# Optimization experiments

Measured on AMD Instinct MI355X. Metric: run time of the kernel, lower is better.

Reference implementation:

```python
import jax, jax.numpy as jnp
import numpy as np

B, L, K, D = 65536, 4, 1024, 512


def setup_inputs() -> dict:
    key = jax.random.key(0)
    k1, k2 = jax.random.split(key)
    z_e = jax.random.normal(k1, (B, D), dtype=jnp.float32)
    # torch init: uniform(-1/codebook_size, 1/codebook_size)
    codebooks = jax.random.uniform(k2, (L, K, D), dtype=jnp.float32,
                                   minval=-1.0 / K, maxval=1.0 / K)
    return {"z_e": z_e, "codebooks": codebooks}


def reference(z_e, codebooks):
    sg = jax.lax.stop_gradient

    def step(carry, cb):
        # carry: (residual [B,D], quantized_sum [B,D], vq_loss scalar); cb: [K,D]
        residual, qsum, loss = carry
        # squared euclidean distances [B,K]
        d2 = (jnp.sum(residual * residual, axis=1, keepdims=True)
              + jnp.sum(cb * cb, axis=1)
              - 2.0 * residual @ cb.T)
        idx = jnp.argmin(d2, axis=1)          # [B]
        q = cb[idx]                           # [B,D] gather
        loss = loss + jnp.mean((q - sg(residual)) ** 2) \
                    + jnp.mean((sg(q) - residual) ** 2)
        return (residual - q, qsum + q, loss), idx

    init = (z_e, jnp.zeros_like(z_e), jnp.float32(0.0))
    (residual, qsum, vq_loss), codes = jax.lax.scan(step, init, codebooks)
    # straight-through estimator
    z_q_st = z_e + sg(qsum - z_e)
    return z_q_st, codes, vq_loss
```

## Files before the change

kernel.cpp:

```cpp
#include <hip/hip_runtime.h>
#include <math.h>

#define NB 65536
#define ND 512
#define NK 1024
#define NL 4
#define THR 1e-3f

typedef __attribute__((ext_vector_type(8))) short short8;
typedef __attribute__((ext_vector_type(4))) float floatx4;

__device__ inline unsigned short bf16_rne(float x) {
  unsigned int u = __float_as_uint(x);
  unsigned int r = u + 0x7FFFu + ((u >> 16) & 1u);
  return (unsigned short)(r >> 16);
}

__global__ void cn_kernel(const float* __restrict__ cb, float* __restrict__ cn) {
  const int code = blockIdx.x;
  const float* row = cb + (size_t)code * ND;
  const int t = threadIdx.x;
  const float x = row[t];
  const float y = row[t + 256];
  double s = (double)x * x + (double)y * y;
  for (int off = 32; off > 0; off >>= 1) s += __shfl_down(s, off);
  __shared__ double part[4];
  if ((t & 63) == 0) part[t >> 6] = s;
  __syncthreads();
  if (t == 0) cn[code] = (float)(part[0] + part[1] + part[2] + part[3]);
}

__global__ void rn_kernel(const float* __restrict__ x, float* __restrict__ rn) {
  const int t = threadIdx.x;
  const int row = blockIdx.x * 2 + (t >> 7);
  const int c = (t & 127) << 2;
  const float4 v = *(const float4*)(x + (size_t)row * ND + c);
  double s = (double)v.x * v.x + (double)v.y * v.y + (double)v.z * v.z + (double)v.w * v.w;
  for (int off = 32; off > 0; off >>= 1) s += __shfl_down(s, off);
  __shared__ double part[4];
  if ((t & 63) == 0) part[t >> 6] = s;
  __syncthreads();
  if ((t & 127) == 0) rn[row] = (float)(part[t >> 6] + part[(t >> 6) + 1]);
}

__global__ __launch_bounds__(512, 2)
void argmin_mfma(const float* __restrict__ res,
                 const float* __restrict__ cb,
                 const float* __restrict__ rn,
                 const float* __restrict__ cn,
                 unsigned int* __restrict__ cnt,
                 unsigned int* __restrict__ cand) {
  __shared__ short A_hi[128][40];
  __shared__ short A_lo[128][40];
  __shared__ short B_hi[256][40];
  __shared__ short B_lo[256][40];
  __shared__ float minbuf[128][4];

  const int t = threadIdx.x;
  const int lane = t & 63;
  const int w = t >> 6;
  const int wr = w >> 2;
  const int wc = w & 3;
  const int q = lane >> 4;
  const int col16 = lane & 15;
  const int rowbase = (blockIdx.x >> 1) * 128;
  const int cbase = (blockIdx.x & 1) * 512;

  const int sa_row = t >> 2, sa_k = (t & 3) * 8;
  const int sb_row = t >> 1, sb_k = (t & 1) * 16;

  for (int nc = 0; nc < 2; ++nc) {
    floatx4 acc[4][4];
#pragma unroll
    for (int i = 0; i < 4; ++i)
#pragma unroll
      for (int j = 0; j < 4; ++j) acc[i][j] = (floatx4){0.f, 0.f, 0.f, 0.f};

    float4 fa0, fa1, fb[4];
    {
      const float* ap = res + (size_t)(rowbase + sa_row) * ND + sa_k;
      fa0 = *(const float4*)(ap);
      fa1 = *(const float4*)(ap + 4);
      const float* bp = cb + (size_t)(cbase + nc * 256 + sb_row) * ND + sb_k;
#pragma unroll
      for (int j = 0; j < 4; ++j) fb[j] = *(const float4*)(bp + 4 * j);
    }

    for (int kc = 0; kc < 16; ++kc) {
      __syncthreads();
      {
        float av[8] = {fa0.x, fa0.y, fa0.z, fa0.w, fa1.x, fa1.y, fa1.z, fa1.w};
        short8 h, l;
#pragma unroll
        for (int j = 0; j < 8; ++j) {
          unsigned short hb = bf16_rne(av[j]);
          float hf = __uint_as_float((unsigned int)hb << 16);
          h[j] = (short)hb;
          l[j] = (short)bf16_rne(av[j] - hf);
        }
        *(short8*)&A_hi[sa_row][sa_k] = h;
        *(short8*)&A_lo[sa_row][sa_k] = l;
        float bv[16];
#pragma unroll
        for (int j = 0; j < 4; ++j) {
          bv[4 * j + 0] = fb[j].x; bv[4 * j + 1] = fb[j].y;
          bv[4 * j + 2] = fb[j].z; bv[4 * j + 3] = fb[j].w;
        }
        short8 h0, l0, h1, l1;
#pragma unroll
        for (int j = 0; j < 8; ++j) {
          unsigned short hb = bf16_rne(bv[j]);
          float hf = __uint_as_float((unsigned int)hb << 16);
          h0[j] = (short)hb;
          l0[j] = (short)bf16_rne(bv[j] - hf);
          unsigned short hb1 = bf16_rne(bv[j + 8]);
          float hf1 = __uint_as_float((unsigned int)hb1 << 16);
          h1[j] = (short)hb1;
          l1[j] = (short)bf16_rne(bv[j + 8] - hf1);
        }
        *(short8*)&B_hi[sb_row][sb_k] = h0;
        *(short8*)&B_lo[sb_row][sb_k] = l0;
        *(short8*)&B_hi[sb_row][sb_k + 8] = h1;
        *(short8*)&B_lo[sb_row][sb_k + 8] = l1;
      }
      __syncthreads();
      if (kc + 1 < 16) {
        const float* ap = res + (size_t)(rowbase + sa_row) * ND + (kc + 1) * 32 + sa_k;
        fa0 = *(const float4*)(ap);
        fa1 = *(const float4*)(ap + 4);
        const float* bp = cb + (size_t)(cbase + nc * 256 + sb_row) * ND + (kc + 1) * 32 + sb_k;
#pragma unroll
        for (int j = 0; j < 4; ++j) fb[j] = *(const float4*)(bp + 4 * j);
      }
      short8 ahi[4], alo[4], bhi[4], blo[4];
#pragma unroll
      for (int ti = 0; ti < 4; ++ti) {
        const int m = wr * 64 + ti * 16 + col16;
        ahi[ti] = *(short8*)&A_hi[m][q * 8];
        alo[ti] = *(short8*)&A_lo[m][q * 8];
      }
#pragma unroll
      for (int tj = 0; tj < 4; ++tj) {
        const int n = wc * 64 + tj * 16 + col16;
        bhi[tj] = *(short8*)&B_hi[n][q * 8];
        blo[tj] = *(short8*)&B_lo[n][q * 8];
      }
#pragma unroll
      for (int ti = 0; ti < 4; ++ti)
#pragma unroll
        for (int tj = 0; tj < 4; ++tj) {
          acc[ti][tj] = __builtin_amdgcn_mfma_f32_16x16x32_bf16(ahi[ti], bhi[tj], acc[ti][tj], 0, 0, 0);
          acc[ti][tj] = __builtin_amdgcn_mfma_f32_16x16x32_bf16(alo[ti], bhi[tj], acc[ti][tj], 0, 0, 0);
          acc[ti][tj] = __builtin_amdgcn_mfma_f32_16x16x32_bf16(ahi[ti], blo[tj], acc[ti][tj], 0, 0, 0);
        }
    }

    float rnv[16], cnv[4];
#pragma unroll
    for (int ti = 0; ti < 4; ++ti)
#pragma unroll
      for (int v = 0; v < 4; ++v)
        rnv[ti * 4 + v] = rn[rowbase + wr * 64 + ti * 16 + q * 4 + v];
#pragma unroll
    for (int tj = 0; tj < 4; ++tj)
      cnv[tj] = cn[cbase + nc * 256 + wc * 64 + tj * 16 + col16];

    float rm[16];
#pragma unroll
    for (int ti = 0; ti < 4; ++ti)
#pragma unroll
      for (int v = 0; v < 4; ++v) {
        float m0 = INFINITY;
#pragma unroll
        for (int tj = 0; tj < 4; ++tj) {
          const float d2 = (rnv[ti * 4 + v] + cnv[tj]) - 2.0f * acc[ti][tj][v];
          m0 = fminf(m0, d2);
        }
        rm[ti * 4 + v] = m0;
      }
#pragma unroll
    for (int mask = 1; mask < 16; mask <<= 1)
#pragma unroll
      for (int i = 0; i < 16; ++i) rm[i] = fminf(rm[i], __shfl_xor(rm[i], mask));
    if (col16 == 0) {
#pragma unroll
      for (int ti = 0; ti < 4; ++ti)
#pragma unroll
        for (int v = 0; v < 4; ++v)
          minbuf[wr * 64 + ti * 16 + q * 4 + v][wc] = rm[ti * 4 + v];
    }
    __syncthreads();
    if (t < 128)
      minbuf[t][0] = fminf(fminf(minbuf[t][0], minbuf[t][1]), fminf(minbuf[t][2], minbuf[t][3]));
    __syncthreads();
#pragma unroll
    for (int ti = 0; ti < 4; ++ti)
#pragma unroll
      for (int v = 0; v < 4; ++v) {
        const int grow = rowbase + wr * 64 + ti * 16 + q * 4 + v;
        const float thrv = minbuf[wr * 64 + ti * 16 + q * 4 + v][0] + THR;
#pragma unroll
        for (int tj = 0; tj < 4; ++tj) {
          const float d2 = (rnv[ti * 4 + v] + cnv[tj]) - 2.0f * acc[ti][tj][v];
          if (d2 <= thrv) {
            const unsigned int gcol = cbase + nc * 256 + wc * 64 + tj * 16 + col16;
            const unsigned int slot = atomicAdd(&cnt[grow], 1u);
            if (slot < 16) cand[(size_t)grow * 16 + slot] = gcol;
          }
        }
      }
    __syncthreads();
  }
}

__global__ __launch_bounds__(256)
void recheck_kernel(const float* __restrict__ res, const float* __restrict__ cb,
                    const float* __restrict__ rn, const float* __restrict__ cn,
                    const unsigned int* __restrict__ cnt,
                    const unsigned int* __restrict__ cand,
                    int* __restrict__ idx) {
  const int t = threadIdx.x;
  const int lane = t & 63;
  const int slot = lane & 3;
  const int row = blockIdx.x * 64 + (t >> 2);
  const int wavebase = blockIdx.x * 64 + (t >> 6) * 16;
  const unsigned int c = cnt[row];
  const float* rp = res + (size_t)row * ND;
  const float rnr = rn[row];

  if (c <= 16) {
    float bestv = INFINITY;
    int bestk = 0x7fffffff;
    for (unsigned int s = slot; s < c; s += 4) {
      const int k = (int)cand[(size_t)row * 16 + s];
      const float* cp = cb + (size_t)k * ND;
      float acc = 0.f;
#pragma unroll 8
      for (int d = 0; d < ND; d += 4) {
        const float4 rv = *(const float4*)(rp + d);
        const float4 cv = *(const float4*)(cp + d);
        acc = fmaf(rv.x, cv.x, acc);
        acc = fmaf(rv.y, cv.y, acc);
        acc = fmaf(rv.z, cv.z, acc);
        acc = fmaf(rv.w, cv.w, acc);
      }
      const float d2 = (rnr + cn[k]) - 2.0f * acc;
      if (d2 < bestv || (d2 == bestv && k < bestk)) { bestv = d2; bestk = k; }
    }
#pragma unroll
    for (int off = 1; off < 4; off <<= 1) {
      const float ov = __shfl_xor(bestv, off);
      const int ok = __shfl_xor(bestk, off);
      if (ov < bestv || (ov == bestv && ok < bestk)) { bestv = ov; bestk = ok; }
    }
    if (slot == 0) idx[row] = bestk;
  }

  unsigned long long ovf = __ballot(slot == 0 && c > 16);
  while (ovf) {
    const int src = (int)__ffsll(ovf) - 1;
    ovf &= ovf - 1;
    const int orow = wavebase + (src >> 2);
    const float* orp = res + (size_t)orow * ND;
    const float ornr = rn[orow];
    float bv = INFINITY;
    int bk = 0x7fffffff;
    for (int kk = 0; kk < NK; kk += 64) {
      const int k = kk + lane;
      const float* cp = cb + (size_t)k * ND;
      float acc = 0.f;
      for (int d = 0; d < ND; d += 4) {
        const float4 rv = *(const float4*)(orp + d);
        const float4 cv = *(const float4*)(cp + d);
        acc = fmaf(rv.x, cv.x, acc);
        acc = fmaf(rv.y, cv.y, acc);
        acc = fmaf(rv.z, cv.z, acc);
        acc = fmaf(rv.w, cv.w, acc);
      }
      const float d2 = (ornr + cn[k]) - 2.0f * acc;
      if (d2 < bv || (d2 == bv && k < bk)) { bv = d2; bk = k; }
    }
    for (int off = 32; off > 0; off >>= 1) {
      const float ov = __shfl_down(bv, off);
      const int ok = __shfl_down(bk, off);
      if (ov < bv || (ov == bv && ok < bk)) { bv = ov; bk = ok; }
    }
    if (lane == 0) idx[orow] = bk;
  }
}

__global__ void update_kernel(const float* __restrict__ res_in,
                              const float* __restrict__ cb,
                              const int* __restrict__ idx,
                              float* __restrict__ res_out,
                              float* __restrict__ codes_out,
                              float* __restrict__ rn_out,
                              double* __restrict__ lacc) {
  const int t = threadIdx.x;
  const int row = blockIdx.x * 2 + (t >> 7);
  const int c = (t & 127) << 2;
  const int k = idx[row];
  const float4 r = *(const float4*)(res_in + (size_t)row * ND + c);
  const float4 q = *(const float4*)(cb + (size_t)k * ND + c);
  float4 nr;
  nr.x = r.x - q.x; nr.y = r.y - q.y; nr.z = r.z - q.z; nr.w = r.w - q.w;
  *(float4*)(res_out + (size_t)row * ND + c) = nr;
  if (c == 0) codes_out[row] = (float)k;
  double s = (double)nr.x * nr.x + (double)nr.y * nr.y +
             (double)nr.z * nr.z + (double)nr.w * nr.w;
  for (int off = 32; off > 0; off >>= 1) s += __shfl_down(s, off);
  __shared__ double part[4];
  if ((t & 63) == 0) part[t >> 6] = s;
  __syncthreads();
  if ((t & 127) == 0) rn_out[row] = (float)(part[t >> 6] + part[(t >> 6) + 1]);
  if (t == 0) atomicAdd(&lacc[blockIdx.x & 511], part[0] + part[1] + part[2] + part[3]);
}

__global__ void loss_reduce(const double* __restrict__ lacc, float* __restrict__ out) {
  const int t = threadIdx.x;
  double s = 0.0;
  for (int i = t; i < NL * 512; i += 256) s += lacc[i];
  for (int off = 32; off > 0; off >>= 1) s += __shfl_down(s, off);
  __shared__ double part[4];
  if ((t & 63) == 0) part[t >> 6] = s;
  __syncthreads();
  if (t == 0)
    out[(size_t)NB * ND + (size_t)NL * NB] =
        (float)(2.0 * (part[0] + part[1] + part[2] + part[3]) / ((double)NB * (double)ND));
}

__global__ void final_kernel(const float* __restrict__ z_e,
                             const float* __restrict__ cbs,
                             float* __restrict__ out) {
  const size_t gid = (size_t)blockIdx.x * 256 + threadIdx.x;
  const int row = (int)(gid >> 7);
  const int c = ((int)gid & 127) << 2;
  const float* codes = out + (size_t)NB * ND;
  const int k0 = (int)codes[0 * NB + row];
  const int k1 = (int)codes[1 * NB + row];
  const int k2 = (int)codes[2 * NB + row];
  const int k3 = (int)codes[3 * NB + row];
  const float4 q0 = *(const float4*)(cbs + ((size_t)0 * NK + k0) * ND + c);
  const float4 q1 = *(const float4*)(cbs + ((size_t)1 * NK + k1) * ND + c);
  const float4 q2 = *(const float4*)(cbs + ((size_t)2 * NK + k2) * ND + c);
  const float4 q3 = *(const float4*)(cbs + ((size_t)3 * NK + k3) * ND + c);
  const float4 z = *(const float4*)(z_e + (size_t)row * ND + c);
  float4 qs, o;
  qs.x = ((q0.x + q1.x) + q2.x) + q3.x;
  qs.y = ((q0.y + q1.y) + q2.y) + q3.y;
  qs.z = ((q0.z + q1.z) + q2.z) + q3.z;
  qs.w = ((q0.w + q1.w) + q2.w) + q3.w;
  o.x = z.x + (qs.x - z.x);
  o.y = z.y + (qs.y - z.y);
  o.z = z.z + (qs.z - z.z);
  o.w = z.w + (qs.w - z.w);
  *(float4*)(out + (size_t)row * ND + c) = o;
}

extern "C" void kernel_launch(void* const* d_in, const int* in_sizes, int n_in,
                              void* d_out, int out_size, void* d_ws, size_t ws_size,
                              hipStream_t stream) {
  const float* z_e = (const float*)d_in[0];
  const float* cbs = (const float*)d_in[1];
  float* out = (float*)d_out;
  char* ws = (char*)d_ws;

  double* lacc = (double*)ws;
  float* rn = (float*)(ws + 16384);
  float* cn = (float*)(ws + 16384 + 262144);
  unsigned int* cnt = (unsigned int*)(ws + 16384 + 262144 + 16384);
  unsigned int* cand = (unsigned int*)(ws + 16384 + 262144 + 16384 + 262144);
  int* idx = (int*)(ws + 16384 + 262144 + 16384 + 262144 + 4194304);

  float* resb = out;
  float* codes = out + (size_t)NB * ND;

  hipMemsetAsync(lacc, 0, NL * 512 * sizeof(double), stream);
  cn_kernel<<<NL * NK, 256, 0, stream>>>(cbs, cn);
  rn_kernel<<<NB / 2, 256, 0, stream>>>(z_e, rn);

  for (int l = 0; l < NL; ++l) {
    const float* rin = (l == 0) ? z_e : resb;
    const float* cbl = cbs + (size_t)l * NK * ND;
    hipMemsetAsync(cnt, 0, (size_t)NB * 4, stream);
    argmin_mfma<<<(NB / 128) * 2, 512, 0, stream>>>(rin, cbl, rn, cn + l * NK, cnt, cand);
    recheck_kernel<<<NB / 64, 256, 0, stream>>>(rin, cbl, rn, cn + l * NK, cnt, cand, idx);
    update_kernel<<<NB / 2, 256, 0, stream>>>(
        rin, cbl, idx, resb, codes + (size_t)l * NB, rn, lacc + (size_t)l * 512);
  }

  loss_reduce<<<1, 256, 0, stream>>>(lacc, out);
  final_kernel<<<(NB * (size_t)ND) / 4 / 256, 256, 0, stream>>>(z_e, cbs, out);
}
```

Before: 2.323 ms.

## Precompute bf16 hi/lo splits of codebook and residual outside the GEMM

Adds a split kernel that converts the codebooks into bf16 hi/lo arrays once. rn_kernel and update_kernel also emit bf16 hi/lo copies of the residual. The argmin MFMA kernel can then load pre-split shorts instead of converting fp32 on every tile. In the original code the codebook tile was re-split by each of the 1024 row blocks, so this removes redundant conversion ALU work and halves-per-array load bytes. The cost is extra workspace, extra writes in update/rn, and a mode choice that depends on the workspace size.

Result: no change. 2.342 ms (+0.8%).

```diff
diff --git a/kernel.cpp b/kernel.cpp
--- a/kernel.cpp
+++ b/kernel.cpp
@@ -8,6 +8,7 @@
 #define THR 1e-3f
 
 typedef __attribute__((ext_vector_type(8))) short short8;
+typedef __attribute__((ext_vector_type(4))) short short4_t;
 typedef __attribute__((ext_vector_type(4))) float floatx4;
 
 __device__ inline unsigned short bf16_rne(float x) {
@@ -30,22 +31,59 @@
   if (t == 0) cn[code] = (float)(part[0] + part[1] + part[2] + part[3]);
 }
 
-__global__ void rn_kernel(const float* __restrict__ x, float* __restrict__ rn) {
+__global__ void split_kernel(const float* __restrict__ x, short* __restrict__ hi,
+                             short* __restrict__ lo) {
+  const size_t i = ((size_t)blockIdx.x * 256 + threadIdx.x) * 4;
+  const float4 v = *(const float4*)(x + i);
+  const float av[4] = {v.x, v.y, v.z, v.w};
+  short4_t h, l;
+#pragma unroll
+  for (int j = 0; j < 4; ++j) {
+    unsigned short hb = bf16_rne(av[j]);
+    float hf = __uint_as_float((unsigned int)hb << 16);
+    h[j] = (short)hb;
+    l[j] = (short)bf16_rne(av[j] - hf);
+  }
+  *(short4_t*)(hi + i) = h;
+  *(short4_t*)(lo + i) = l;
+}
+
+__global__ void rn_kernel(const float* __restrict__ x, float* __restrict__ rn,
+                          short* __restrict__ rh, short* __restrict__ rl, int do_split) {
   const int t = threadIdx.x;
   const int row = blockIdx.x * 2 + (t >> 7);
   const int c = (t & 127) << 2;
-  const float4 v = *(const float4*)(x + (size_t)row * ND + c);
+  const size_t off = (size_t)row * ND + c;
+  const float4 v = *(const float4*)(x + off);
+  if (do_split) {
+    const float av[4] = {v.x, v.y, v.z, v.w};
+    short4_t h, l;
+#pragma unroll
+    for (int j = 0; j < 4; ++j) {
+      unsigned short hb = bf16_rne(av[j]);
+      float hf = __uint_as_float((unsigned int)hb << 16);
+      h[j] = (short)hb;
+      l[j] = (short)bf16_rne(av[j] - hf);
+    }
+    *(short4_t*)(rh + off) = h;
+    *(short4_t*)(rl + off) = l;
+  }
   double s = (double)v.x * v.x + (double)v.y * v.y + (double)v.z * v.z + (double)v.w * v.w;
-  for (int off = 32; off > 0; off >>= 1) s += __shfl_down(s, off);
+  for (int off2 = 32; off2 > 0; off2 >>= 1) s += __shfl_down(s, off2);
   __shared__ double part[4];
   if ((t & 63) == 0) part[t >> 6] = s;
   __syncthreads();
   if ((t & 127) == 0) rn[row] = (float)(part[t >> 6] + part[(t >> 6) + 1]);
 }
 
+template <int MODE>
 __global__ __launch_bounds__(512, 2)
 void argmin_mfma(const float* __restrict__ res,
+                 const short* __restrict__ rh,
+                 const short* __restrict__ rl,
                  const float* __restrict__ cb,
+                 const short* __restrict__ cbh,
+                 const short* __restrict__ cbl,
                  const float* __restrict__ rn,
                  const float* __restrict__ cn,
                  unsigned int* __restrict__ cnt,
@@ -77,18 +115,36 @@
       for (int j = 0; j < 4; ++j) acc[i][j] = (floatx4){0.f, 0.f, 0.f, 0.f};
 
     float4 fa0, fa1, fb[4];
+    short8 pah, pal, pbh0, pbh1, pbl0, pbl1;
     {
-      const float* ap = res + (size_t)(rowbase + sa_row) * ND + sa_k;
-      fa0 = *(const float4*)(ap);
-      fa1 = *(const float4*)(ap + 4);
-      const float* bp = cb + (size_t)(cbase + nc * 256 + sb_row) * ND + sb_k;
-#pragma unroll
-      for (int j = 0; j < 4; ++j) fb[j] = *(const float4*)(bp + 4 * j);
+      if constexpr (MODE == 2) {
+        const size_t aoff = (size_t)(rowbase + sa_row) * ND + sa_k;
+        pah = *(const short8*)(rh + aoff);
+        pal = *(const short8*)(rl + aoff);
+      } else {
+        const float* ap = res + (size_t)(rowbase + sa_row) * ND + sa_k;
+        fa0 = *(const float4*)(ap);
+        fa1 = *(const float4*)(ap + 4);
+      }
+      if constexpr (MODE >= 1) {
+        const size_t boff = (size_t)(cbase + nc * 256 + sb_row) * ND + sb_k;
+        pbh0 = *(const short8*)(cbh + boff);
+        pbh1 = *(const short8*)(cbh + boff + 8);
+        pbl0 = *(const short8*)(cbl + boff);
+        pbl1 = *(const short8*)(cbl + boff + 8);
+      } else {
+        const float* bp = cb + (size_t)(cbase + nc * 256 + sb_row) * ND + sb_k;
+#pragma unroll
+        for (int j = 0; j < 4; ++j) fb[j] = *(const float4*)(bp + 4 * j);
+      }
     }
 
     for (int kc = 0; kc < 16; ++kc) {
       __syncthreads();
-      {
+      if constexpr (MODE == 2) {
+        *(short8*)&A_hi[sa_row][sa_k] = pah;
+        *(short8*)&A_lo[sa_row][sa_k] = pal;
+      } else {
         float av[8] = {fa0.x, fa0.y, fa0.z, fa0.w, fa1.x, fa1.y, fa1.z, fa1.w};
         short8 h, l;
 #pragma unroll
@@ -100,6 +156,13 @@
         }
         *(short8*)&A_hi[sa_row][sa_k] = h;
         *(short8*)&A_lo[sa_row][sa_k] = l;
+      }
+      if constexpr (MODE >= 1) {
+        *(short8*)&B_hi[sb_row][sb_k] = pbh0;
+        *(short8*)&B_hi[sb_row][sb_k + 8] = pbh1;
+        *(short8*)&B_lo[sb_row][sb_k] = pbl0;
+        *(short8*)&B_lo[sb_row][sb_k + 8] = pbl1;
+      } else {
         float bv[16];
 #pragma unroll
         for (int j = 0; j < 4; ++j) {
@@ -125,12 +188,28 @@
       }
       __syncthreads();
       if (kc + 1 < 16) {
-        const float* ap = res + (size_t)(rowbase + sa_row) * ND + (kc + 1) * 32 + sa_k;
-        fa0 = *(const float4*)(ap);
-        fa1 = *(const float4*)(ap + 4);
-        const float* bp = cb + (size_t)(cbase + nc * 256 + sb_row) * ND + (kc + 1) * 32 + sb_k;
-#pragma unroll
-        for (int j = 0; j < 4; ++j) fb[j] = *(const float4*)(bp + 4 * j);
+        if constexpr (MODE == 2) {
+          const size_t aoff = (size_t)(rowbase + sa_row) * ND + (kc + 1) * 32 + sa_k;
+          pah = *(const short8*)(rh + aoff);
+          pal = *(const short8*)(rl + aoff);
+        } else {
+          const float* ap = res + (size_t)(rowbase + sa_row) * ND + (kc + 1) * 32 + sa_k;
+          fa0 = *(const float4*)(ap);
+          fa1 = *(const float4*)(ap + 4);
+        }
+        if constexpr (MODE >= 1) {
+          const size_t boff =
+              (size_t)(cbase + nc * 256 + sb_row) * ND + (kc + 1) * 32 + sb_k;
+          pbh0 = *(const short8*)(cbh + boff);
+          pbh1 = *(const short8*)(cbh + boff + 8);
+          pbl0 = *(const short8*)(cbl + boff);
+          pbl1 = *(const short8*)(cbl + boff + 8);
+        } else {
+          const float* bp =
+              cb + (size_t)(cbase + nc * 256 + sb_row) * ND + (kc + 1) * 32 + sb_k;
+#pragma unroll
+          for (int j = 0; j < 4; ++j) fb[j] = *(const float4*)(bp + 4 * j);
+        }
       }
       short8 ahi[4], alo[4], bhi[4], blo[4];
 #pragma unroll
@@ -295,20 +374,36 @@
                               float* __restrict__ res_out,
                               float* __restrict__ codes_out,
                               float* __restrict__ rn_out,
-                              double* __restrict__ lacc) {
+                              double* __restrict__ lacc,
+                              short* __restrict__ rh, short* __restrict__ rl,
+                              int do_split) {
   const int t = threadIdx.x;
   const int row = blockIdx.x * 2 + (t >> 7);
   const int c = (t & 127) << 2;
   const int k = idx[row];
-  const float4 r = *(const float4*)(res_in + (size_t)row * ND + c);
+  const size_t off = (size_t)row * ND + c;
+  const float4 r = *(const float4*)(res_in + off);
   const float4 q = *(const float4*)(cb + (size_t)k * ND + c);
   float4 nr;
   nr.x = r.x - q.x; nr.y = r.y - q.y; nr.z = r.z - q.z; nr.w = r.w - q.w;
-  *(float4*)(res_out + (size_t)row * ND + c) = nr;
+  *(float4*)(res_out + off) = nr;
+  if (do_split) {
+    const float av[4] = {nr.x, nr.y, nr.z, nr.w};
+    short4_t h, l;
+#pragma unroll
+    for (int j = 0; j < 4; ++j) {
+      unsigned short hb = bf16_rne(av[j]);
+      float hf = __uint_as_float((unsigned int)hb << 16);
+      h[j] = (short)hb;
+      l[j] = (short)bf16_rne(av[j] - hf);
+    }
+    *(short4_t*)(rh + off) = h;
+    *(short4_t*)(rl + off) = l;
+  }
   if (c == 0) codes_out[row] = (float)k;
   double s = (double)nr.x * nr.x + (double)nr.y * nr.y +
              (double)nr.z * nr.z + (double)nr.w * nr.w;
-  for (int off = 32; off > 0; off >>= 1) s += __shfl_down(s, off);
+  for (int off2 = 32; off2 > 0; off2 >>= 1) s += __shfl_down(s, off2);
   __shared__ double part[4];
   if ((t & 63) == 0) part[t >> 6] = s;
   __syncthreads();
@@ -365,28 +460,61 @@
   float* out = (float*)d_out;
   char* ws = (char*)d_ws;
 
+  const size_t OFF_RN   = 16384;
+  const size_t OFF_CN   = OFF_RN + 262144;
+  const size_t OFF_CNT  = OFF_CN + 16384;
+  const size_t OFF_CAND = OFF_CNT + 262144;
+  const size_t OFF_IDX  = OFF_CAND + 4194304;
+  const size_t OFF_CBH  = OFF_IDX + 262144;
+  const size_t OFF_CBL  = OFF_CBH + (size_t)NL * NK * ND * 2;
+  const size_t OFF_RH   = OFF_CBL + (size_t)NL * NK * ND * 2;
+  const size_t OFF_RL   = OFF_RH + (size_t)NB * ND * 2;
+  const size_t WS_MODE1 = OFF_RH;
+  const size_t WS_MODE2 = OFF_RL + (size_t)NB * ND * 2;
+
   double* lacc = (double*)ws;
-  float* rn = (float*)(ws + 16384);
-  float* cn = (float*)(ws + 16384 + 262144);
-  unsigned int* cnt = (unsigned int*)(ws + 16384 + 262144 + 16384);
-  unsigned int* cand = (unsigned int*)(ws + 16384 + 262144 + 16384 + 262144);
-  int* idx = (int*)(ws + 16384 + 262144 + 16384 + 262144 + 4194304);
+  float* rn = (float*)(ws + OFF_RN);
+  float* cn = (float*)(ws + OFF_CN);
+  unsigned int* cnt = (unsigned int*)(ws + OFF_CNT);
+  unsigned int* cand = (unsigned int*)(ws + OFF_CAND);
+  int* idx = (int*)(ws + OFF_IDX);
+  short* cb_hi = (short*)(ws + OFF_CBH);
+  short* cb_lo = (short*)(ws + OFF_CBL);
+  short* res_hi = (short*)(ws + OFF_RH);
+  short* res_lo = (short*)(ws + OFF_RL);
+
+  int mode = 0;
+  if (ws_size >= WS_MODE2) mode = 2;
+  else if (ws_size >= WS_MODE1) mode = 1;
 
   float* resb = out;
   float* codes = out + (size_t)NB * ND;
 
   hipMemsetAsync(lacc, 0, NL * 512 * sizeof(double), stream);
   cn_kernel<<<NL * NK, 256, 0, stream>>>(cbs, cn);
-  rn_kernel<<<NB / 2, 256, 0, stream>>>(z_e, rn);
+  if (mode >= 1)
+    split_kernel<<<(NL * NK * ND) / 1024, 256, 0, stream>>>(cbs, cb_hi, cb_lo);
+  rn_kernel<<<NB / 2, 256, 0, stream>>>(z_e, rn, res_hi, res_lo, mode == 2 ? 1 : 0);
 
   for (int l = 0; l < NL; ++l) {
     const float* rin = (l == 0) ? z_e : resb;
-    const float* cbl = cbs + (size_t)l * NK * ND;
+    const float* cbl_f = cbs + (size_t)l * NK * ND;
+    const short* cblh = cb_hi + (size_t)l * NK * ND;
+    const short* cbll = cb_lo + (size_t)l * NK * ND;
     hipMemsetAsync(cnt, 0, (size_t)NB * 4, stream);
-    argmin_mfma<<<(NB / 128) * 2, 512, 0, stream>>>(rin, cbl, rn, cn + l * NK, cnt, cand);
-    recheck_kernel<<<NB / 64, 256, 0, stream>>>(rin, cbl, rn, cn + l * NK, cnt, cand, idx);
+    if (mode == 2)
+      argmin_mfma<2><<<(NB / 128) * 2, 512, 0, stream>>>(
+          rin, res_hi, res_lo, cbl_f, cblh, cbll, rn, cn + l * NK, cnt, cand);
+    else if (mode == 1)
+      argmin_mfma<1><<<(NB / 128) * 2, 512, 0, stream>>>(
+          rin, nullptr, nullptr, cbl_f, cblh, cbll, rn, cn + l * NK, cnt, cand);
+    else
+      argmin_mfma<0><<<(NB / 128) * 2, 512, 0, stream>>>(
+          rin, nullptr, nullptr, cbl_f, nullptr, nullptr, rn, cn + l * NK, cnt, cand);
+    recheck_kernel<<<NB / 64, 256, 0, stream>>>(rin, cbl_f, rn, cn + l * NK, cnt, cand, idx);
     update_kernel<<<NB / 2, 256, 0, stream>>>(
-        rin, cbl, idx, resb, codes + (size_t)l * NB, rn, lacc + (size_t)l * 512);
+        rin, cbl_f, idx, resb, codes + (size_t)l * NB, rn, lacc + (size_t)l * 512,
+        res_hi, res_lo, (mode == 2 && l < NL - 1) ? 1 : 0);
   }
 
   loss_reduce<<<1, 256, 0, stream>>>(lacc, out);
```
